# Optimization experiments

Measured on AMD Instinct MI355X. Metric: run time of the kernel, lower is better.

The kernel has to match this reference:

```python
import jax, jax.numpy as jnp
import numpy as np

N, E, SEQ, IN, HID, OUT = 2048, 65536, 5, 32, 64, 16
EPS = 1e-5


def setup_inputs() -> dict:
    ks = jax.random.split(jax.random.key(0), 16)
    def w(k, shape):
        return jax.random.normal(k, shape, jnp.float32) / np.float32(np.sqrt(shape[0]))
    z = lambda n: jnp.zeros((n,), jnp.float32)
    return dict(
        x=jax.random.normal(ks[0], (SEQ, N, IN), jnp.float32),
        edge_weight=jax.random.uniform(ks[1], (E,), jnp.float32),
        Wcz=w(ks[2], (IN, HID)), bcz=z(HID), Wlz=w(ks[3], (2 * HID, HID)), blz=z(HID),
        Wcr=w(ks[4], (IN, HID)), bcr=z(HID), Wlr=w(ks[5], (2 * HID, HID)), blr=z(HID),
        Wch=w(ks[6], (IN, HID)), bch=z(HID), Wlh=w(ks[7], (2 * HID, HID)), blh=z(HID),
        Wred=w(ks[8], (SEQ * HID, HID)), bred=z(HID),
        Wc1=w(ks[9], (HID, HID)), bc1=z(HID), Wc2=w(ks[10], (HID, HID)), bc2=z(HID),
        g1=jnp.ones((HID,), jnp.float32), be1=z(HID),
        g2=jnp.ones((HID,), jnp.float32), be2=z(HID),
        Wout=w(ks[11], (HID, OUT)), bout=z(OUT),
        Wi1=w(ks[12], (2 * HID, HID)), bi1=z(HID),
        Wi2=w(ks[13], (HID, 1)), bi2=z(1),
        edge_index=jax.random.randint(ks[14], (2, E), 0, N),
    )


def _layer_norm(h, g, b):
    mu = jnp.mean(h, -1, keepdims=True)
    var = jnp.mean((h - mu) ** 2, -1, keepdims=True)
    return (h - mu) * jax.lax.rsqrt(var + EPS) * g + b


def _forward(x, edge_weight, Wcz, bcz, Wlz, blz, Wcr, bcr, Wlr, blr,
             Wch, bch, Wlh, blh, Wred, bred, Wc1, bc1, Wc2, bc2,
             g1, be1, g2, be2, Wout, bout, Wi1, bi1, Wi2, bi2, edge_index):
    src, dst = edge_index[0], edge_index[1]
    # GCN symmetric normalization with self-loops (weight 1.0); shared by all convs.
    deg = jax.ops.segment_sum(edge_weight, dst, num_segments=N) + 1.0
    dinv = jax.lax.rsqrt(deg)
    norm = dinv[src] * edge_weight * dinv[dst]  # [E]
    dself = dinv * dinv                          # [N] self-loop coefficient

    def gcn(h, W, b):
        hw = h @ W
        agg = jax.ops.segment_sum(norm[:, None] * hw[src], dst, num_segments=N)
        return agg + dself[:, None] * hw + b

    # TGCN per timestep. The original passes no hidden state, so H resets to 0
    # each call: H_t = (1 - Z) * tanh(candidate); reset gate R is multiplied by
    # H=0 and has no effect (its params get zero gradient, matching torch).
    hs = []
    for t in range(SEQ):  # SEQ=5, fixed small loop
        Zg = jax.nn.sigmoid(gcn(x[t], Wcz, bcz) @ Wlz[:HID] + blz)
        Ht = jnp.tanh(gcn(x[t], Wch, bch) @ Wlh[:HID] + blh)
        hs.append((1.0 - Zg) * Ht)
    h = jnp.stack(hs, axis=1).reshape(N, SEQ * HID)
    h = h @ Wred + bred
    emb = h  # intermediate embeddings for the interaction predictor
    h = gcn(h, Wc1, bc1)
    h = jax.nn.relu(_layer_norm(h, g1, be1))  # dropout = identity in eval
    h = gcn(h, Wc2, bc2)
    h = jax.nn.relu(_layer_norm(h, g2, be2))
    node_pred = h @ Wout + bout
    # InteractionPredictor: cat([e_i, e_j]) @ Wi1 == e_i @ Wi1[:H] + e_j @ Wi1[H:]
    a = emb @ Wi1[:HID]
    bj = emb @ Wi1[HID:]
    hp = jax.nn.relu(a[:, None, :] + bj[None, :, :] + bi1)  # [N, N, HID]
    scores = (hp @ Wi2)[..., 0] + bi2[0]                     # [N, N]
    return node_pred, scores


def reference(x, edge_index, edge_weight, Wcz, bcz, Wlz, blz, Wcr, bcr, Wlr, blr,
              Wch, bch, Wlh, blh, Wred, bred, Wc1, bc1, Wc2, bc2,
              g1, be1, g2, be2, Wout, bout, Wi1, bi1, Wi2, bi2):
    return _forward(x, edge_weight, Wcz, bcz, Wlz, blz, Wcr, bcr, Wlr, blr,
                    Wch, bch, Wlh, blh, Wred, bred, Wc1, bc1, Wc2, bc2,
                    g1, be1, g2, be2, Wout, bout, Wi1, bi1, Wi2, bi2, edge_index)
```

## Files before the change

### kernel.cpp

```cpp
#include <hip/hip_runtime.h>
#include <math.h>

#define N_NODES 2048
#define N_EDGES 65536
#define SEQL 5
#define IN_F 32
#define HID 64
#define OUT_F 16
#define LN_EPS 1e-5f
#define CAP 128

__global__ __launch_bounds__(256) void k_build(
        const int* __restrict__ ei, const float* __restrict__ ew,
        const float* __restrict__ Wcz, const float* __restrict__ Wlz,
        const float* __restrict__ bcz, const float* __restrict__ blz,
        const float* __restrict__ Wch, const float* __restrict__ Wlh,
        const float* __restrict__ bch, const float* __restrict__ blh,
        int* __restrict__ cnt, float2* __restrict__ cedge,
        float* __restrict__ Wzp, float* __restrict__ Whp, float* __restrict__ bUV){
    int b = blockIdx.x, t = threadIdx.x;
    if (b < 256){
        int e = b * 256 + t;
        int s = ei[e], d = ei[N_EDGES + e];
        int pos = atomicAdd(&cnt[d], 1);
        if (pos < CAP){
            float2 v;
            v.x = __int_as_float(s);
            v.y = ew[e];
            cedge[(d << 7) + pos] = v;
        }
    } else {
        const float* Wc = (b == 256) ? Wcz : Wch;
        const float* Wl = (b == 256) ? Wlz : Wlh;
        const float* bc = (b == 256) ? bcz : bch;
        const float* bl = (b == 256) ? blz : blh;
        float* Wp = (b == 256) ? Wzp : Whp;
        for (int idx = t; idx < IN_F*HID; idx += 256){
            int i = idx >> 6, f = idx & 63;
            float s = 0.f;
            #pragma unroll 8
            for (int k = 0; k < HID; ++k) s += Wc[i*HID+k] * Wl[k*HID+f];
            Wp[idx] = s;
        }
        if (t < HID){
            float s = bl[t];
            for (int k = 0; k < HID; ++k) s += bc[k] * Wl[k*HID+t];
            bUV[(b-256)*HID + t] = s;
        }
    }
}

__global__ void k_dinv(const int* __restrict__ cnt, const float2* __restrict__ cedge,
                       float* __restrict__ dinv, float* __restrict__ dself){
    int n = blockIdx.x * 64 + threadIdx.x;
    int m = min(cnt[n], CAP);
    float s = 1.f;
    for (int i = 0; i < m; ++i) s += cedge[(n << 7) + i].y;
    float iv = 1.f / sqrtf(s);
    dinv[n] = iv;
    dself[n] = iv * iv;
}

__global__ __launch_bounds__(320) void k_gate(const float* __restrict__ x,
        const float* __restrict__ dinv, const float* __restrict__ dself,
        const int* __restrict__ cnt, const float2* __restrict__ cedge,
        const float* __restrict__ bUV, const float* __restrict__ Wzp, const float* __restrict__ Whp,
        const float* __restrict__ Wred, const float* __restrict__ bred,
        const float* __restrict__ Wi1, const float* __restrict__ bi1, const float* __restrict__ Wc1,
        float* __restrict__ ag, float* __restrict__ bjp, float* __restrict__ hw1y){
    int n = blockIdx.x;
    int tid = threadIdx.x;
    __shared__ float part[40*SEQL*IN_F];
    __shared__ float axs[SEQL][IN_F];
    __shared__ float hs[SEQL][HID];
    __shared__ float pw[SEQL][HID];
    __shared__ float hemb[HID];
    const int slot = tid >> 3, fl = tid & 7;
    const int f = tid & 63, t = tid >> 6;
    int m = min(cnt[n], CAP);
    float dvn = dinv[n], dsn = dself[n];
    const float4* X4 = (const float4*)x;
    float4 a0 = {0,0,0,0}, a1 = {0,0,0,0}, a2 = {0,0,0,0}, a3 = {0,0,0,0}, a4 = {0,0,0,0};
    for (int p = slot; p < m; p += 40){
        float2 ed = cedge[(n << 7) + p];
        int s = __float_as_int(ed.x);
        float c = ed.y * dinv[s];
        float4 x0 = X4[(0*N_NODES + s)*8 + fl];
        float4 x1 = X4[(1*N_NODES + s)*8 + fl];
        float4 x2 = X4[(2*N_NODES + s)*8 + fl];
        float4 x3 = X4[(3*N_NODES + s)*8 + fl];
        float4 x4v= X4[(4*N_NODES + s)*8 + fl];
        a0.x += c*x0.x; a0.y += c*x0.y; a0.z += c*x0.z; a0.w += c*x0.w;
        a1.x += c*x1.x; a1.y += c*x1.y; a1.z += c*x1.z; a1.w += c*x1.w;
        a2.x += c*x2.x; a2.y += c*x2.y; a2.z += c*x2.z; a2.w += c*x2.w;
        a3.x += c*x3.x; a3.y += c*x3.y; a3.z += c*x3.z; a3.w += c*x3.w;
        a4.x += c*x4v.x; a4.y += c*x4v.y; a4.z += c*x4v.z; a4.w += c*x4v.w;
    }
    *(float4*)&part[(slot*SEQL + 0)*IN_F + fl*4] = a0;
    *(float4*)&part[(slot*SEQL + 1)*IN_F + fl*4] = a1;
    *(float4*)&part[(slot*SEQL + 2)*IN_F + fl*4] = a2;
    *(float4*)&part[(slot*SEQL + 3)*IN_F + fl*4] = a3;
    *(float4*)&part[(slot*SEQL + 4)*IN_F + fl*4] = a4;
    __syncthreads();
    if (tid < SEQL*IN_F){
        int tt = tid >> 5, ff = tid & 31;
        float ps = 0.f;
        #pragma unroll 8
        for (int sl = 0; sl < 40; ++sl) ps += part[(sl*SEQL + tt)*IN_F + ff];
        axs[tt][ff] = dsn * x[(tt*N_NODES + n)*IN_F + ff] + dvn * ps;
    }
    __syncthreads();
    {
        float zz = bUV[f], hh = bUV[HID + f];
        #pragma unroll
        for (int i = 0; i < IN_F; ++i){
            float a = axs[t][i];
            zz += a * Wzp[i*HID + f];
            hh += a * Whp[i*HID + f];
        }
        float z = 1.f / (1.f + expf(-zz));
        hs[t][f] = (1.f - z) * tanhf(hh);
    }
    __syncthreads();
    {   float pp = 0.f;
        #pragma unroll
        for (int k = 0; k < HID; ++k) pp += hs[t][k] * Wred[(t*HID + k)*HID + f];
        pw[t][f] = pp;
    }
    __syncthreads();
    if (tid < HID){
        float hr = bred[tid];
        #pragma unroll
        for (int t2 = 0; t2 < SEQL; ++t2) hr += pw[t2][tid];
        hemb[tid] = hr;
    }
    __syncthreads();
    if (t < 3){
        const float* W = (t == 0) ? Wi1 : (t == 1) ? (Wi1 + HID*HID) : Wc1;
        float acc = (t == 1) ? bi1[f] : 0.f;
        #pragma unroll
        for (int k = 0; k < HID; ++k) acc += hemb[k] * W[k*HID + f];
        if (t == 2) acc *= dvn;
        float* O = (t == 0) ? ag : (t == 1) ? bjp : hw1y;
        O[n*HID + f] = acc;
    }
}

__global__ __launch_bounds__(512) void k_gcn1s(
        const float* __restrict__ hw1y, const float* __restrict__ dinv,
        const int* __restrict__ cnt, const float2* __restrict__ cedge,
        const float* __restrict__ bc1, const float* __restrict__ g1, const float* __restrict__ be1,
        const float* __restrict__ Wc2, float* __restrict__ hw2y,
        const float* __restrict__ ag, const float* __restrict__ bjp,
        const float* __restrict__ Wi2, const float* __restrict__ bi2,
        float* __restrict__ outs){
    int blk = blockIdx.x;
    int tid = threadIdx.x;
    if (blk < 256){
        int w = tid >> 6, l = tid & 63;
        int n = (blk << 3) + w;
        int slot = l >> 4, fl = l & 15;
        int m = min(cnt[n], CAP);
        float dv = dinv[n];
        const float4* H4 = (const float4*)hw1y;
        float4 acc = {0.f,0.f,0.f,0.f};
        if (slot == 0) acc = H4[n*16 + fl];
        for (int p = slot; p < m; p += 4){
            float2 ed = cedge[(n << 7) + p];
            int s = __float_as_int(ed.x); float c = ed.y;
            float4 h = H4[s*16 + fl];
            acc.x += c*h.x; acc.y += c*h.y; acc.z += c*h.z; acc.w += c*h.w;
        }
        acc.x += __shfl_xor(acc.x, 16); acc.y += __shfl_xor(acc.y, 16);
        acc.z += __shfl_xor(acc.z, 16); acc.w += __shfl_xor(acc.w, 16);
        acc.x += __shfl_xor(acc.x, 32); acc.y += __shfl_xor(acc.y, 32);
        acc.z += __shfl_xor(acc.z, 32); acc.w += __shfl_xor(acc.w, 32);
        float4 b4 = ((const float4*)bc1)[fl];
        float4 g;
        g.x = b4.x + dv*acc.x; g.y = b4.y + dv*acc.y;
        g.z = b4.z + dv*acc.z; g.w = b4.w + dv*acc.w;
        float s4 = g.x + g.y + g.z + g.w;
        s4 += __shfl_xor(s4, 1); s4 += __shfl_xor(s4, 2);
        s4 += __shfl_xor(s4, 4); s4 += __shfl_xor(s4, 8);
        float mu = s4 * (1.f/64.f);
        float4 d;
        d.x = g.x - mu; d.y = g.y - mu; d.z = g.z - mu; d.w = g.w - mu;
        float v4 = d.x*d.x + d.y*d.y + d.z*d.z + d.w*d.w;
        v4 += __shfl_xor(v4, 1); v4 += __shfl_xor(v4, 2);
        v4 += __shfl_xor(v4, 4); v4 += __shfl_xor(v4, 8);
        float rs = 1.f / sqrtf(v4 * (1.f/64.f) + LN_EPS);
        float4 gm = ((const float4*)g1)[fl], be = ((const float4*)be1)[fl];
        float4 h4;
        h4.x = fmaxf(d.x*rs*gm.x + be.x, 0.f);
        h4.y = fmaxf(d.y*rs*gm.y + be.y, 0.f);
        h4.z = fmaxf(d.z*rs*gm.z + be.z, 0.f);
        h4.w = fmaxf(d.w*rs*gm.w + be.w, 0.f);
        float o = 0.f;
        #pragma unroll 4
        for (int gk = 0; gk < 16; ++gk){
            float hb0 = __shfl(h4.x, gk);
            float hb1 = __shfl(h4.y, gk);
            float hb2 = __shfl(h4.z, gk);
            float hb3 = __shfl(h4.w, gk);
            o += hb0 * Wc2[(4*gk+0)*HID + l];
            o += hb1 * Wc2[(4*gk+1)*HID + l];
            o += hb2 * Wc2[(4*gk+2)*HID + l];
            o += hb3 * Wc2[(4*gk+3)*HID + l];
        }
        hw2y[n*HID + l] = dv * o;
    } else {
        __shared__ float bs[64*65];
        __shared__ float wv[64];
        int tl = blk - 256;
        int j0 = (tl & 31) * 64;
        int i0 = (tl >> 5) * 32;
        for (int idx = tid; idx < 4096; idx += 512){
            int jj = idx >> 6, f = idx & 63;
            bs[jj*65 + f] = bjp[(j0 + jj)*HID + f];
        }
        if (tid < 64) wv[tid] = Wi2[tid];
        __syncthreads();
        int tj = tid & 63;
        int w = __builtin_amdgcn_readfirstlane(tid >> 6);
        const float* ar = ag + (i0 + w*4)*HID;
        float bi2v = bi2[0];
        float acc0 = 0.f, acc1 = 0.f, acc2 = 0.f, acc3 = 0.f;
        #pragma unroll
        for (int f = 0; f < 64; ++f){
            float bv = bs[tj*65 + f];
            float wf = wv[f];
            acc0 += fmaxf(ar[       f] + bv, 0.f) * wf;
            acc1 += fmaxf(ar[ 64 +  f] + bv, 0.f) * wf;
            acc2 += fmaxf(ar[128 +  f] + bv, 0.f) * wf;
            acc3 += fmaxf(ar[192 +  f] + bv, 0.f) * wf;
        }
        long ro = (long)(i0 + w*4) * N_NODES + j0 + tj;
        outs[ro                ] = acc0 + bi2v;
        outs[ro +     N_NODES  ] = acc1 + bi2v;
        outs[ro + 2L* N_NODES  ] = acc2 + bi2v;
        outs[ro + 3L* N_NODES  ] = acc3 + bi2v;
    }
}

__global__ __launch_bounds__(512) void k_gcn2s(
        const float* __restrict__ hw2y, const float* __restrict__ dinv,
        const int* __restrict__ cnt, const float2* __restrict__ cedge,
        const float* __restrict__ bc2, const float* __restrict__ g2, const float* __restrict__ be2,
        const float* __restrict__ Wout, const float* __restrict__ bout,
        const float* __restrict__ ag, const float* __restrict__ bjp,
        const float* __restrict__ Wi2, const float* __restrict__ bi2,
        float* __restrict__ outp, float* __restrict__ outs){
    int blk = blockIdx.x;
    int tid = threadIdx.x;
    if (blk < 256){
        int w = tid >> 6, l = tid & 63;
        int n = (blk << 3) + w;
        int slot = l >> 4, fl = l & 15;
        int m = min(cnt[n], CAP);
        float dv = dinv[n];
        const float4* H4 = (const float4*)hw2y;
        float4 acc = {0.f,0.f,0.f,0.f};
        if (slot == 0) acc = H4[n*16 + fl];
        for (int p = slot; p < m; p += 4){
            float2 ed = cedge[(n << 7) + p];
            int s = __float_as_int(ed.x); float c = ed.y;
            float4 h = H4[s*16 + fl];
            acc.x += c*h.x; acc.y += c*h.y; acc.z += c*h.z; acc.w += c*h.w;
        }
        acc.x += __shfl_xor(acc.x, 16); acc.y += __shfl_xor(acc.y, 16);
        acc.z += __shfl_xor(acc.z, 16); acc.w += __shfl_xor(acc.w, 16);
        acc.x += __shfl_xor(acc.x, 32); acc.y += __shfl_xor(acc.y, 32);
        acc.z += __shfl_xor(acc.z, 32); acc.w += __shfl_xor(acc.w, 32);
        float4 b4 = ((const float4*)bc2)[fl];
        float4 g;
        g.x = b4.x + dv*acc.x; g.y = b4.y + dv*acc.y;
        g.z = b4.z + dv*acc.z; g.w = b4.w + dv*acc.w;
        float s4 = g.x + g.y + g.z + g.w;
        s4 += __shfl_xor(s4, 1); s4 += __shfl_xor(s4, 2);
        s4 += __shfl_xor(s4, 4); s4 += __shfl_xor(s4, 8);
        float mu = s4 * (1.f/64.f);
        float4 d;
        d.x = g.x - mu; d.y = g.y - mu; d.z = g.z - mu; d.w = g.w - mu;
        float v4 = d.x*d.x + d.y*d.y + d.z*d.z + d.w*d.w;
        v4 += __shfl_xor(v4, 1); v4 += __shfl_xor(v4, 2);
        v4 += __shfl_xor(v4, 4); v4 += __shfl_xor(v4, 8);
        float rs = 1.f / sqrtf(v4 * (1.f/64.f) + LN_EPS);
        float4 gm = ((const float4*)g2)[fl], be = ((const float4*)be2)[fl];
        float4 h4;
        h4.x = fmaxf(d.x*rs*gm.x + be.x, 0.f);
        h4.y = fmaxf(d.y*rs*gm.y + be.y, 0.f);
        h4.z = fmaxf(d.z*rs*gm.z + be.z, 0.f);
        h4.w = fmaxf(d.w*rs*gm.w + be.w, 0.f);
        int f2 = l & 15;
        float o = bout[f2];
        #pragma unroll 4
        for (int gk = 0; gk < 16; ++gk){
            float hb0 = __shfl(h4.x, gk);
            float hb1 = __shfl(h4.y, gk);
            float hb2 = __shfl(h4.z, gk);
            float hb3 = __shfl(h4.w, gk);
            o += hb0 * Wout[(4*gk+0)*OUT_F + f2];
            o += hb1 * Wout[(4*gk+1)*OUT_F + f2];
            o += hb2 * Wout[(4*gk+2)*OUT_F + f2];
            o += hb3 * Wout[(4*gk+3)*OUT_F + f2];
        }
        if (slot == 0) outp[n*OUT_F + f2] = o;
    } else {
        __shared__ float bs[64*65];
        __shared__ float wv[64];
        int tl = blk - 256 + 1024;
        int j0 = (tl & 31) * 64;
        int i0 = (tl >> 5) * 32;
        for (int idx = tid; idx < 4096; idx += 512){
            int jj = idx >> 6, f = idx & 63;
            bs[jj*65 + f] = bjp[(j0 + jj)*HID + f];
        }
        if (tid < 64) wv[tid] = Wi2[tid];
        __syncthreads();
        int tj = tid & 63;
        int w = __builtin_amdgcn_readfirstlane(tid >> 6);
        const float* ar = ag + (i0 + w*4)*HID;
        float bi2v = bi2[0];
        float acc0 = 0.f, acc1 = 0.f, acc2 = 0.f, acc3 = 0.f;
        #pragma unroll
        for (int f = 0; f < 64; ++f){
            float bv = bs[tj*65 + f];
            float wf = wv[f];
            acc0 += fmaxf(ar[       f] + bv, 0.f) * wf;
            acc1 += fmaxf(ar[ 64 +  f] + bv, 0.f) * wf;
            acc2 += fmaxf(ar[128 +  f] + bv, 0.f) * wf;
            acc3 += fmaxf(ar[192 +  f] + bv, 0.f) * wf;
        }
        long ro = (long)(i0 + w*4) * N_NODES + j0 + tj;
        outs[ro                ] = acc0 + bi2v;
        outs[ro +     N_NODES  ] = acc1 + bi2v;
        outs[ro + 2L* N_NODES  ] = acc2 + bi2v;
        outs[ro + 3L* N_NODES  ] = acc3 + bi2v;
    }
}

extern "C" void kernel_launch(void* const* d_in, const int* in_sizes, int n_in,
                              void* d_out, int out_size, void* d_ws, size_t ws_size,
                              hipStream_t stream){
    const float* x   = (const float*)d_in[0];
    const float* ew  = (const float*)d_in[1];
    const float* Wcz = (const float*)d_in[2];  const float* bcz = (const float*)d_in[3];
    const float* Wlz = (const float*)d_in[4];  const float* blz = (const float*)d_in[5];
    const float* Wch = (const float*)d_in[10]; const float* bch = (const float*)d_in[11];
    const float* Wlh = (const float*)d_in[12]; const float* blh = (const float*)d_in[13];
    const float* Wred= (const float*)d_in[14]; const float* bred= (const float*)d_in[15];
    const float* Wc1 = (const float*)d_in[16]; const float* bc1 = (const float*)d_in[17];
    const float* Wc2 = (const float*)d_in[18]; const float* bc2 = (const float*)d_in[19];
    const float* g1  = (const float*)d_in[20]; const float* be1 = (const float*)d_in[21];
    const float* g2  = (const float*)d_in[22]; const float* be2 = (const float*)d_in[23];
    const float* Wout= (const float*)d_in[24]; const float* bout= (const float*)d_in[25];
    const float* Wi1 = (const float*)d_in[26]; const float* bi1 = (const float*)d_in[27];
    const float* Wi2 = (const float*)d_in[28]; const float* bi2 = (const float*)d_in[29];
    const int*  ei  = (const int*)d_in[30];

    float* w = (float*)d_ws;
    int*   cnt   = (int*)w;
    float* dinv  = w + 2048;
    float* dself = w + 4096;
    float2* cedge= (float2*)(w + 6144);
    float* Wzp   = w + 530432;
    float* Whp   = w + 532480;
    float* bUV   = w + 534528;
    float* ag    = w + 534656;
    float* bjp   = w + 665728;
    float* hw1y  = w + 796800;
    float* hw2y  = w + 927872;

    hipMemsetAsync(cnt, 0, 8192, stream);
    k_build<<<258, 256, 0, stream>>>(ei, ew, Wcz, Wlz, bcz, blz, Wch, Wlh, bch, blh,
                                     cnt, cedge, Wzp, Whp, bUV);
    k_dinv<<<32, 64, 0, stream>>>(cnt, cedge, dinv, dself);
    k_gate<<<N_NODES, 320, 0, stream>>>(x, dinv, dself, cnt, cedge, bUV, Wzp, Whp,
                                        Wred, bred, Wi1, bi1, Wc1, ag, bjp, hw1y);
    k_gcn1s<<<256 + 1024, 512, 0, stream>>>(hw1y, dinv, cnt, cedge, bc1, g1, be1,
                                            Wc2, hw2y, ag, bjp, Wi2, bi2,
                                            (float*)d_out + N_NODES*OUT_F);
    k_gcn2s<<<256 + 1024, 512, 0, stream>>>(hw2y, dinv, cnt, cedge, bc2, g2, be2,
                                            Wout, bout, ag, bjp, Wi2, bi2,
                                            (float*)d_out, (float*)d_out + N_NODES*OUT_F);
}
```

Before: 203.9 us.

## Fold degree computation into edge build and run gate kernel one wavefront per node

Edge-weight degrees are now accumulated with float atomics inside the edge-build kernel, which removes the separate dinv kernel and its launch. Each consumer recomputes the inverse square root from the degree array. The gate kernel is restructured so that one 64-lane wavefront handles one node, four nodes per block. It replaces the shared-memory partial sums and block barriers with register accumulators and cross-lane shuffles through the gate, reduction and projection stages. Tradeoffs are float atomic contention on degrees, non-deterministic summation order, and more register pressure from five per-timestep accumulators.

```diff
diff --git a/kernel.cpp b/kernel.cpp
--- a/kernel.cpp
+++ b/kernel.cpp
@@ -16,17 +16,19 @@
         const float* __restrict__ bcz, const float* __restrict__ blz,
         const float* __restrict__ Wch, const float* __restrict__ Wlh,
         const float* __restrict__ bch, const float* __restrict__ blh,
-        int* __restrict__ cnt, float2* __restrict__ cedge,
+        float* __restrict__ deg, int* __restrict__ cnt, float2* __restrict__ cedge,
         float* __restrict__ Wzp, float* __restrict__ Whp, float* __restrict__ bUV){
     int b = blockIdx.x, t = threadIdx.x;
     if (b < 256){
         int e = b * 256 + t;
         int s = ei[e], d = ei[N_EDGES + e];
+        float wv = ew[e];
+        atomicAdd(&deg[d], wv);
         int pos = atomicAdd(&cnt[d], 1);
         if (pos < CAP){
             float2 v;
             v.x = __int_as_float(s);
-            v.y = ew[e];
+            v.y = wv;
             cedge[(d << 7) + pos] = v;
         }
     } else {
@@ -50,104 +52,81 @@
     }
 }
 
-__global__ void k_dinv(const int* __restrict__ cnt, const float2* __restrict__ cedge,
-                       float* __restrict__ dinv, float* __restrict__ dself){
-    int n = blockIdx.x * 64 + threadIdx.x;
-    int m = min(cnt[n], CAP);
-    float s = 1.f;
-    for (int i = 0; i < m; ++i) s += cedge[(n << 7) + i].y;
-    float iv = 1.f / sqrtf(s);
-    dinv[n] = iv;
-    dself[n] = iv * iv;
-}
-
-__global__ __launch_bounds__(320) void k_gate(const float* __restrict__ x,
-        const float* __restrict__ dinv, const float* __restrict__ dself,
-        const int* __restrict__ cnt, const float2* __restrict__ cedge,
+__global__ __launch_bounds__(256) void k_gate(const float* __restrict__ x,
+        const float* __restrict__ deg, const int* __restrict__ cnt,
+        const float2* __restrict__ cedge,
         const float* __restrict__ bUV, const float* __restrict__ Wzp, const float* __restrict__ Whp,
         const float* __restrict__ Wred, const float* __restrict__ bred,
         const float* __restrict__ Wi1, const float* __restrict__ bi1, const float* __restrict__ Wc1,
         float* __restrict__ ag, float* __restrict__ bjp, float* __restrict__ hw1y){
-    int n = blockIdx.x;
     int tid = threadIdx.x;
-    __shared__ float part[40*SEQL*IN_F];
-    __shared__ float axs[SEQL][IN_F];
-    __shared__ float hs[SEQL][HID];
-    __shared__ float pw[SEQL][HID];
-    __shared__ float hemb[HID];
-    const int slot = tid >> 3, fl = tid & 7;
-    const int f = tid & 63, t = tid >> 6;
+    int w = tid >> 6, l = tid & 63;
+    int n = (blockIdx.x << 2) + w;
+    int el = l >> 5, f = l & 31;
     int m = min(cnt[n], CAP);
-    float dvn = dinv[n], dsn = dself[n];
-    const float4* X4 = (const float4*)x;
-    float4 a0 = {0,0,0,0}, a1 = {0,0,0,0}, a2 = {0,0,0,0}, a3 = {0,0,0,0}, a4 = {0,0,0,0};
-    for (int p = slot; p < m; p += 40){
-        float2 ed = cedge[(n << 7) + p];
+    float dvn = 1.f / sqrtf(deg[n] + 1.f);
+    float dsn = dvn * dvn;
+    const float2* ce = cedge + (n << 7);
+    float a0=0.f, a1=0.f, a2=0.f, a3=0.f, a4=0.f;
+    for (int p = el; p < m; p += 2){
+        float2 ed = ce[p];
         int s = __float_as_int(ed.x);
-        float c = ed.y * dinv[s];
-        float4 x0 = X4[(0*N_NODES + s)*8 + fl];
-        float4 x1 = X4[(1*N_NODES + s)*8 + fl];
-        float4 x2 = X4[(2*N_NODES + s)*8 + fl];
-        float4 x3 = X4[(3*N_NODES + s)*8 + fl];
-        float4 x4v= X4[(4*N_NODES + s)*8 + fl];
-        a0.x += c*x0.x; a0.y += c*x0.y; a0.z += c*x0.z; a0.w += c*x0.w;
-        a1.x += c*x1.x; a1.y += c*x1.y; a1.z += c*x1.z; a1.w += c*x1.w;
-        a2.x += c*x2.x; a2.y += c*x2.y; a2.z += c*x2.z; a2.w += c*x2.w;
-        a3.x += c*x3.x; a3.y += c*x3.y; a3.z += c*x3.z; a3.w += c*x3.w;
-        a4.x += c*x4v.x; a4.y += c*x4v.y; a4.z += c*x4v.z; a4.w += c*x4v.w;
-    }
-    *(float4*)&part[(slot*SEQL + 0)*IN_F + fl*4] = a0;
-    *(float4*)&part[(slot*SEQL + 1)*IN_F + fl*4] = a1;
-    *(float4*)&part[(slot*SEQL + 2)*IN_F + fl*4] = a2;
-    *(float4*)&part[(slot*SEQL + 3)*IN_F + fl*4] = a3;
-    *(float4*)&part[(slot*SEQL + 4)*IN_F + fl*4] = a4;
-    __syncthreads();
-    if (tid < SEQL*IN_F){
-        int tt = tid >> 5, ff = tid & 31;
-        float ps = 0.f;
-        #pragma unroll 8
-        for (int sl = 0; sl < 40; ++sl) ps += part[(sl*SEQL + tt)*IN_F + ff];
-        axs[tt][ff] = dsn * x[(tt*N_NODES + n)*IN_F + ff] + dvn * ps;
-    }
-    __syncthreads();
-    {
-        float zz = bUV[f], hh = bUV[HID + f];
-        #pragma unroll
-        for (int i = 0; i < IN_F; ++i){
-            float a = axs[t][i];
-            zz += a * Wzp[i*HID + f];
-            hh += a * Whp[i*HID + f];
-        }
-        float z = 1.f / (1.f + expf(-zz));
-        hs[t][f] = (1.f - z) * tanhf(hh);
-    }
-    __syncthreads();
-    {   float pp = 0.f;
-        #pragma unroll
-        for (int k = 0; k < HID; ++k) pp += hs[t][k] * Wred[(t*HID + k)*HID + f];
-        pw[t][f] = pp;
-    }
-    __syncthreads();
-    if (tid < HID){
-        float hr = bred[tid];
-        #pragma unroll
-        for (int t2 = 0; t2 < SEQL; ++t2) hr += pw[t2][tid];
-        hemb[tid] = hr;
-    }
-    __syncthreads();
-    if (t < 3){
-        const float* W = (t == 0) ? Wi1 : (t == 1) ? (Wi1 + HID*HID) : Wc1;
-        float acc = (t == 1) ? bi1[f] : 0.f;
-        #pragma unroll
-        for (int k = 0; k < HID; ++k) acc += hemb[k] * W[k*HID + f];
-        if (t == 2) acc *= dvn;
-        float* O = (t == 0) ? ag : (t == 1) ? bjp : hw1y;
-        O[n*HID + f] = acc;
-    }
+        float c = ed.y * (1.f / sqrtf(deg[s] + 1.f));
+        a0 += c * x[(0*N_NODES + s)*IN_F + f];
+        a1 += c * x[(1*N_NODES + s)*IN_F + f];
+        a2 += c * x[(2*N_NODES + s)*IN_F + f];
+        a3 += c * x[(3*N_NODES + s)*IN_F + f];
+        a4 += c * x[(4*N_NODES + s)*IN_F + f];
+    }
+    a0 += __shfl_xor(a0, 32); a1 += __shfl_xor(a1, 32); a2 += __shfl_xor(a2, 32);
+    a3 += __shfl_xor(a3, 32); a4 += __shfl_xor(a4, 32);
+    a0 = dsn * x[(0*N_NODES + n)*IN_F + f] + dvn * a0;
+    a1 = dsn * x[(1*N_NODES + n)*IN_F + f] + dvn * a1;
+    a2 = dsn * x[(2*N_NODES + n)*IN_F + f] + dvn * a2;
+    a3 = dsn * x[(3*N_NODES + n)*IN_F + f] + dvn * a3;
+    a4 = dsn * x[(4*N_NODES + n)*IN_F + f] + dvn * a4;
+    float bz = bUV[l], bh = bUV[HID + l];
+    float z0=bz, z1=bz, z2=bz, z3=bz, z4=bz;
+    float h0=bh, h1=bh, h2=bh, h3=bh, h4=bh;
+    #pragma unroll
+    for (int i = 0; i < IN_F; ++i){
+        float wz = Wzp[i*HID + l];
+        float wh = Whp[i*HID + l];
+        float b0 = __shfl(a0, i), b1 = __shfl(a1, i), b2 = __shfl(a2, i);
+        float b3 = __shfl(a3, i), b4 = __shfl(a4, i);
+        z0 += b0*wz; z1 += b1*wz; z2 += b2*wz; z3 += b3*wz; z4 += b4*wz;
+        h0 += b0*wh; h1 += b1*wh; h2 += b2*wh; h3 += b3*wh; h4 += b4*wh;
+    }
+    float s0 = 1.f/(1.f+expf(-z0)), s1 = 1.f/(1.f+expf(-z1)), s2 = 1.f/(1.f+expf(-z2));
+    float s3 = 1.f/(1.f+expf(-z3)), s4 = 1.f/(1.f+expf(-z4));
+    h0 = (1.f-s0)*tanhf(h0); h1 = (1.f-s1)*tanhf(h1); h2 = (1.f-s2)*tanhf(h2);
+    h3 = (1.f-s3)*tanhf(h3); h4 = (1.f-s4)*tanhf(h4);
+    float pw = bred[l];
+    #pragma unroll
+    for (int k = 0; k < HID; ++k){
+        float b0 = __shfl(h0, k), b1 = __shfl(h1, k), b2 = __shfl(h2, k);
+        float b3 = __shfl(h3, k), b4 = __shfl(h4, k);
+        pw += b0 * Wred[(0*HID + k)*HID + l];
+        pw += b1 * Wred[(1*HID + k)*HID + l];
+        pw += b2 * Wred[(2*HID + k)*HID + l];
+        pw += b3 * Wred[(3*HID + k)*HID + l];
+        pw += b4 * Wred[(4*HID + k)*HID + l];
+    }
+    float aA = 0.f, aB = bi1[l], aC = 0.f;
+    #pragma unroll
+    for (int k = 0; k < HID; ++k){
+        float hb = __shfl(pw, k);
+        aA += hb * Wi1[k*HID + l];
+        aB += hb * Wi1[HID*HID + k*HID + l];
+        aC += hb * Wc1[k*HID + l];
+    }
+    ag  [n*HID + l] = aA;
+    bjp [n*HID + l] = aB;
+    hw1y[n*HID + l] = dvn * aC;
 }
 
 __global__ __launch_bounds__(512) void k_gcn1s(
-        const float* __restrict__ hw1y, const float* __restrict__ dinv,
+        const float* __restrict__ hw1y, const float* __restrict__ deg,
         const int* __restrict__ cnt, const float2* __restrict__ cedge,
         const float* __restrict__ bc1, const float* __restrict__ g1, const float* __restrict__ be1,
         const float* __restrict__ Wc2, float* __restrict__ hw2y,
@@ -161,7 +140,7 @@
         int n = (blk << 3) + w;
         int slot = l >> 4, fl = l & 15;
         int m = min(cnt[n], CAP);
-        float dv = dinv[n];
+        float dv = 1.f / sqrtf(deg[n] + 1.f);
         const float4* H4 = (const float4*)hw1y;
         float4 acc = {0.f,0.f,0.f,0.f};
         if (slot == 0) acc = H4[n*16 + fl];
@@ -243,7 +222,7 @@
 }
 
 __global__ __launch_bounds__(512) void k_gcn2s(
-        const float* __restrict__ hw2y, const float* __restrict__ dinv,
+        const float* __restrict__ hw2y, const float* __restrict__ deg,
         const int* __restrict__ cnt, const float2* __restrict__ cedge,
         const float* __restrict__ bc2, const float* __restrict__ g2, const float* __restrict__ be2,
         const float* __restrict__ Wout, const float* __restrict__ bout,
@@ -257,7 +236,7 @@
         int n = (blk << 3) + w;
         int slot = l >> 4, fl = l & 15;
         int m = min(cnt[n], CAP);
-        float dv = dinv[n];
+        float dv = 1.f / sqrtf(deg[n] + 1.f);
         const float4* H4 = (const float4*)hw2y;
         float4 acc = {0.f,0.f,0.f,0.f};
         if (slot == 0) acc = H4[n*16 + fl];
@@ -359,28 +338,26 @@
     const int*  ei  = (const int*)d_in[30];
 
     float* w = (float*)d_ws;
-    int*   cnt   = (int*)w;
-    float* dinv  = w + 2048;
-    float* dself = w + 4096;
-    float2* cedge= (float2*)(w + 6144);
-    float* Wzp   = w + 530432;
-    float* Whp   = w + 532480;
-    float* bUV   = w + 534528;
-    float* ag    = w + 534656;
-    float* bjp   = w + 665728;
-    float* hw1y  = w + 796800;
-    float* hw2y  = w + 927872;
-
-    hipMemsetAsync(cnt, 0, 8192, stream);
+    float* deg   = w;
+    int*   cnt   = (int*)(w + 2048);
+    float2* cedge= (float2*)(w + 4096);
+    float* Wzp   = w + 528384;
+    float* Whp   = w + 530432;
+    float* bUV   = w + 532480;
+    float* ag    = w + 532608;
+    float* bjp   = w + 663680;
+    float* hw1y  = w + 794752;
+    float* hw2y  = w + 925824;
+
+    hipMemsetAsync(deg, 0, 16384, stream);
     k_build<<<258, 256, 0, stream>>>(ei, ew, Wcz, Wlz, bcz, blz, Wch, Wlh, bch, blh,
-                                     cnt, cedge, Wzp, Whp, bUV);
-    k_dinv<<<32, 64, 0, stream>>>(cnt, cedge, dinv, dself);
-    k_gate<<<N_NODES, 320, 0, stream>>>(x, dinv, dself, cnt, cedge, bUV, Wzp, Whp,
-                                        Wred, bred, Wi1, bi1, Wc1, ag, bjp, hw1y);
-    k_gcn1s<<<256 + 1024, 512, 0, stream>>>(hw1y, dinv, cnt, cedge, bc1, g1, be1,
+                                     deg, cnt, cedge, Wzp, Whp, bUV);
+    k_gate<<<512, 256, 0, stream>>>(x, deg, cnt, cedge, bUV, Wzp, Whp,
+                                    Wred, bred, Wi1, bi1, Wc1, ag, bjp, hw1y);
+    k_gcn1s<<<256 + 1024, 512, 0, stream>>>(hw1y, deg, cnt, cedge, bc1, g1, be1,
                                             Wc2, hw2y, ag, bjp, Wi2, bi2,
                                             (float*)d_out + N_NODES*OUT_F);
-    k_gcn2s<<<256 + 1024, 512, 0, stream>>>(hw2y, dinv, cnt, cedge, bc2, g2, be2,
+    k_gcn2s<<<256 + 1024, 512, 0, stream>>>(hw2y, deg, cnt, cedge, bc2, g2, be2,
                                             Wout, bout, ag, bjp, Wi2, bi2,
                                             (float*)d_out, (float*)d_out + N_NODES*OUT_F);
 }
```

After: 326.0 us. 1.6x slower.
